# Kernel tuning notes

Measured on AMD Instinct MI355X. Metric: run time of the kernel, lower is better.

The kernel has to match this reference:

```python
import jax, jax.numpy as jnp
import numpy as np

D, H, O, E, TOPK = 1024, 4096, 1024, 8, 2
B, L = 2, 2048
ROUTE_SCALE = 1.0


def setup_inputs() -> dict:
    key = jax.random.key(0)
    ks = jax.random.split(key, 7)
    # xavier-uniform bound for gate weight (E, D)
    gb = float(np.sqrt(6.0 / (E + D)))
    return {
        "x": jax.random.normal(ks[0], (B, L, D), dtype=jnp.float32),
        "gate_w": jax.random.uniform(ks[1], (E, D), jnp.float32, -gb, gb),
        "gate_b": jnp.zeros((E,), jnp.float32),
        "w1": jax.random.normal(ks[2], (E, D, H), jnp.float32) * 0.02,
        "b1": jnp.zeros((E, H), jnp.float32),
        "w2": jax.random.normal(ks[3], (E, H, O), jnp.float32) * 0.02,
        "b2": jnp.zeros((E, O), jnp.float32),
    }


def reference(x, gate_w, gate_b, w1, b1, w2, b2):
    Bb, Ll, Dd = x.shape
    N = Bb * Ll
    x_flat = x.reshape(N, Dd)  # (N, D)

    # ---- Gate: softmax router + top-k ----
    logits = x_flat @ gate_w.T + gate_b              # (N, E)
    probs = jax.nn.softmax(logits * ROUTE_SCALE, axis=-1)
    topk_vals, topk_idx = jax.lax.top_k(probs, TOPK)  # (N, K)

    # dense gate: zeros except selected experts keep their prob
    dense_gate = jnp.zeros((N, E), probs.dtype).at[
        jnp.arange(N)[:, None], topk_idx
    ].set(topk_vals)                                  # (N, E)

    # ---- Experts (vectorized over E; gate weights are exactly zero for
    #      non-selected experts, so the combine reproduces the sparse
    #      gather-MLP-scatter math of the original loop) ----
    h = jax.nn.relu(jnp.einsum("nd,edh->neh", x_flat, w1) + b1)  # (N, E, H)
    y = jnp.einsum("neh,eho->neo", h, w2) + b2                   # (N, E, O)
    out_flat = jnp.einsum("ne,neo->no", dense_gate, y)           # (N, O)

    return out_flat.reshape(Bb, Ll, O)
```

## Files before the change

### kernel.cpp

```cpp
#include <hip/hip_runtime.h>
#include <hip/hip_bf16.h>
#include <stdint.h>

#define NTOK 4096
#define DDIM 1024
#define HDIM 4096
#define ODIM 1024
#define NEXP 8
#define BM 256
#define BN 256
#define BK 64
#define CAPROWS (NTOK * 2 + NEXP * BM)
#define MAXTILES (CAPROWS / BM)

typedef float f32x4_t __attribute__((ext_vector_type(4)));
typedef short bf16x8_t __attribute__((ext_vector_type(8)));
using bf16_t = __hip_bfloat16;

#define S_BARRIER()                         \
  do {                                      \
    __builtin_amdgcn_sched_barrier(0);      \
    __builtin_amdgcn_s_barrier();           \
    __builtin_amdgcn_sched_barrier(0);      \
  } while (0)
#define WAIT_LGKM0()                                  \
  do {                                                \
    asm volatile("s_waitcnt lgkmcnt(0)" ::: "memory");\
    __builtin_amdgcn_sched_barrier(0);                \
  } while (0)
#define WAIT_VMCNT(n)                                       \
  do {                                                      \
    asm volatile("s_waitcnt vmcnt(" #n ")" ::: "memory");   \
    __builtin_amdgcn_sched_barrier(0);                      \
  } while (0)

__device__ __forceinline__ void gll16(const void* g, void* l) {
  __builtin_amdgcn_global_load_lds(
      (__attribute__((address_space(1))) void*)(void*)g,
      (__attribute__((address_space(3))) void*)l, 16, 0, 0);
}

__global__ __launch_bounds__(256) void gate_kernel(
    const float* __restrict__ x, const float* __restrict__ gw,
    const float* __restrict__ gb, int* __restrict__ top_idx,
    float* __restrict__ top_val, int* __restrict__ counts) {
  int n = blockIdx.x * 4 + (threadIdx.x >> 6);
  int l = threadIdx.x & 63;
  const float4* xv = (const float4*)(x + (size_t)n * DDIM);
  float4 xs[4];
#pragma unroll
  for (int j = 0; j < 4; ++j) xs[j] = xv[l + 64 * j];
  float part[NEXP];
#pragma unroll
  for (int e = 0; e < NEXP; ++e) {
    const float4* wv = (const float4*)(gw + (size_t)e * DDIM);
    float s = 0.f;
#pragma unroll
    for (int j = 0; j < 4; ++j) {
      float4 w4 = wv[l + 64 * j];
      s += xs[j].x * w4.x + xs[j].y * w4.y + xs[j].z * w4.z + xs[j].w * w4.w;
    }
    part[e] = s;
  }
#pragma unroll
  for (int off = 32; off > 0; off >>= 1)
#pragma unroll
    for (int e = 0; e < NEXP; ++e) part[e] += __shfl_xor(part[e], off, 64);

  float m = -1e30f;
#pragma unroll
  for (int e = 0; e < NEXP; ++e) { part[e] += gb[e]; m = fmaxf(m, part[e]); }
  float ssum = 0.f;
#pragma unroll
  for (int e = 0; e < NEXP; ++e) { part[e] = expf(part[e] - m); ssum += part[e]; }
  int i0 = 0; float v0 = part[0];
#pragma unroll
  for (int e = 1; e < NEXP; ++e) if (part[e] > v0) { v0 = part[e]; i0 = e; }
  int i1 = -1; float v1 = -1e30f;
#pragma unroll
  for (int e = 0; e < NEXP; ++e) if (e != i0 && part[e] > v1) { v1 = part[e]; i1 = e; }
  if (l == 0) {
    float inv = 1.f / ssum;
    top_idx[n * 2] = i0; top_idx[n * 2 + 1] = i1;
    top_val[n * 2] = v0 * inv; top_val[n * 2 + 1] = v1 * inv;
    atomicAdd(&counts[i0], 1); atomicAdd(&counts[i1], 1);
  }
}

__global__ void plan_kernel(const int* __restrict__ counts, int* __restrict__ offs,
                            int* __restrict__ tile_e, int* __restrict__ tile_r) {
  if (threadIdx.x != 0 || blockIdx.x != 0) return;
  int off = 0, t = 0;
  for (int e = 0; e < NEXP; ++e) {
    offs[e] = off;
    int padded = ((counts[e] + BM - 1) / BM) * BM;
    for (int r = 0; r < padded; r += BM) { tile_e[t] = e; tile_r[t] = off + r; ++t; }
    off += padded;
  }
  offs[NEXP] = off;
  for (; t < MAXTILES; ++t) { tile_e[t] = -1; tile_r[t] = 0; }
}

__global__ __launch_bounds__(128) void gather_kernel(
    const float* __restrict__ x, const int* __restrict__ top_idx,
    const int* __restrict__ offs, int* __restrict__ cursors,
    int* __restrict__ slot_for, bf16_t* __restrict__ Xg) {
  int a = blockIdx.x;
  __shared__ int s_slot;
  if (threadIdx.x == 0) {
    int e = top_idx[a];
    int pos = atomicAdd(&cursors[e], 1);
    int slot = offs[e] + pos;
    slot_for[a] = slot;
    s_slot = slot;
  }
  __syncthreads();
  int slot = s_slot;
  int n = a >> 1;
  const float4* xv = (const float4*)(x + (size_t)n * DDIM);
  float4 a0 = xv[threadIdx.x * 2], a1 = xv[threadIdx.x * 2 + 1];
  __align__(16) bf16_t tmp[8] = {
      __float2bfloat16(a0.x), __float2bfloat16(a0.y),
      __float2bfloat16(a0.z), __float2bfloat16(a0.w),
      __float2bfloat16(a1.x), __float2bfloat16(a1.y),
      __float2bfloat16(a1.z), __float2bfloat16(a1.w)};
  *(uint4*)(Xg + (size_t)slot * DDIM + threadIdx.x * 8) = *(const uint4*)tmp;
}

__global__ __launch_bounds__(256) void convT_kernel(
    const float* __restrict__ src, bf16_t* __restrict__ dst, int R, int C) {
  __shared__ float tile[64][65];
  int e = blockIdx.z;
  int c0 = blockIdx.x * 64, r0 = blockIdx.y * 64;
  const float* s = src + ((size_t)e * R + r0) * C + c0;
  int tc = threadIdx.x & 63, tr = threadIdx.x >> 6;
#pragma unroll
  for (int p = 0; p < 16; ++p) {
    int r = tr + p * 4;
    tile[r][tc] = s[(size_t)r * C + tc];
  }
  __syncthreads();
  bf16_t* dcol = dst + ((size_t)e * C + c0) * R + r0;
  int t = threadIdx.x;
#pragma unroll
  for (int it = 0; it < 2; ++it) {
    int c = (t >> 3) + it * 32;
    int r8 = (t & 7) * 8;
    __align__(16) bf16_t v[8];
#pragma unroll
    for (int j = 0; j < 8; ++j) v[j] = __float2bfloat16(tile[r8 + j][c]);
    *(uint4*)(dcol + (size_t)c * R + r8) = *(const uint4*)v;
  }
}

template <int KTOT, int NTOT, int WHICH>
__global__ __launch_bounds__(512, 2) void gemm8_kernel(
    const bf16_t* __restrict__ A, const bf16_t* __restrict__ Bt,
    const float* __restrict__ bias, void* __restrict__ Cout,
    const int* __restrict__ tile_e, const int* __restrict__ tile_r) {
  constexpr int NCOL = NTOT / BN;
  int nwg = gridDim.x;
  int bid = blockIdx.x;
  int q = nwg >> 3, rr = nwg & 7;
  int xcd = bid & 7, pos = bid >> 3;
  int swz = (xcd < rr ? xcd * (q + 1) : rr * (q + 1) + (xcd - rr) * q) + pos;
  int ty = swz / NCOL, tx = swz % NCOL;

  int e = tile_e[ty];
  if (e < 0) return;
  int row0 = tile_r[ty];
  int n0 = tx * BN;

  __shared__ char smem[131072];
  int tid = threadIdx.x;
  int w = tid >> 6, l = tid & 63;
  int wm = w >> 2, wn = w & 3;
  int lrow = l & 15, lk = l >> 4;

  const bf16_t* Ab = A + (size_t)row0 * KTOT;
  const bf16_t* Bb = Bt + ((size_t)e * NTOT + n0) * KTOT;

  int sidx0 = tid, sidx1 = 512 + tid;
  int sr0 = sidx0 >> 3, sc0 = (sidx0 & 7) ^ (sr0 & 7);
  int sr1 = sidx1 >> 3, sc1 = (sidx1 & 7) ^ (sr1 & 7);

  auto stageA = [&](int kt, int h, int d) {
    char* lb = smem + d * 32768 + h * 16384;
    const bf16_t* g = Ab + (size_t)(h * 128) * KTOT + kt * BK;
    gll16(g + (size_t)sr0 * KTOT + sc0 * 8, lb + sidx0 * 16);
    gll16(g + (size_t)sr1 * KTOT + sc1 * 8, lb + sidx1 * 16);
  };
  auto stageB = [&](int kt, int h, int d) {
    char* lb = smem + 65536 + d * 32768 + h * 16384;
    const bf16_t* g = Bb + (size_t)(h * 128) * KTOT + kt * BK;
    gll16(g + (size_t)sr0 * KTOT + sc0 * 8, lb + sidx0 * 16);
    gll16(g + (size_t)sr1 * KTOT + sc1 * 8, lb + sidx1 * 16);
  };

  int abase = (wm * 128 + lrow) * 128;
  int bbase = (wn * 64 + lrow) * 128;
  int p0 = ((lk) ^ (lrow & 7)) * 16;
  int p1 = ((4 + lk) ^ (lrow & 7)) * 16;

  f32x4_t acc[8][4];
#pragma unroll
  for (int m = 0; m < 8; ++m)
#pragma unroll
    for (int n = 0; n < 4; ++n) acc[m][n] = (f32x4_t){0.f, 0.f, 0.f, 0.f};

  const int NKT = KTOT / BK;

  stageA(0, 0, 0); stageA(0, 1, 0);
  stageB(0, 0, 0); stageB(0, 1, 0);
  stageA(1, 0, 1); stageA(1, 1, 1);
  WAIT_VMCNT(4);
  S_BARRIER();

  for (int t = 0; t < NKT; ++t) {
    int d = t & 1;
    const char* Ad = smem + d * 32768;
    const char* Bd = smem + 65536 + d * 32768;
    bf16x8_t ak0[8], ak1[8], bv[4];
#pragma unroll
    for (int m = 0; m < 8; ++m)
      ak0[m] = *(const bf16x8_t*)(Ad + abase + m * 2048 + p0);
#pragma unroll
    for (int n = 0; n < 4; ++n)
      bv[n] = *(const bf16x8_t*)(Bd + bbase + n * 2048 + p0);
    if (t + 1 < NKT) stageB(t + 1, 0, d ^ 1);
    S_BARRIER();
    WAIT_LGKM0();
    __builtin_amdgcn_s_setprio(1);
#pragma unroll
    for (int m = 0; m < 4; ++m)
#pragma unroll
      for (int n = 0; n < 4; ++n)
        acc[m][n] = __builtin_amdgcn_mfma_f32_16x16x32_bf16(ak0[m], bv[n], acc[m][n], 0, 0, 0);
    __builtin_amdgcn_s_setprio(0);
    S_BARRIER();
#pragma unroll
    for (int m = 0; m < 8; ++m)
      ak1[m] = *(const bf16x8_t*)(Ad + abase + m * 2048 + p1);
    if (t + 1 < NKT) stageB(t + 1, 1, d ^ 1);
    S_BARRIER();
    WAIT_LGKM0();
    __builtin_amdgcn_s_setprio(1);
#pragma unroll
    for (int m = 4; m < 8; ++m)
#pragma unroll
      for (int n = 0; n < 4; ++n)
        acc[m][n] = __builtin_amdgcn_mfma_f32_16x16x32_bf16(ak0[m], bv[n], acc[m][n], 0, 0, 0);
    __builtin_amdgcn_s_setprio(0);
    S_BARRIER();
#pragma unroll
    for (int n = 0; n < 4; ++n)
      bv[n] = *(const bf16x8_t*)(Bd + bbase + n * 2048 + p1);
    if (t + 2 < NKT) stageA(t + 2, 0, d);
    S_BARRIER();
    WAIT_LGKM0();
    __builtin_amdgcn_s_setprio(1);
#pragma unroll
    for (int m = 0; m < 4; ++m)
#pragma unroll
      for (int n = 0; n < 4; ++n)
        acc[m][n] = __builtin_amdgcn_mfma_f32_16x16x32_bf16(ak1[m], bv[n], acc[m][n], 0, 0, 0);
    __builtin_amdgcn_s_setprio(0);
    S_BARRIER();
    if (t + 2 < NKT) {
      stageA(t + 2, 1, d);
      WAIT_VMCNT(4);
    } else {
      WAIT_VMCNT(0);
    }
    S_BARRIER();
    __builtin_amdgcn_s_setprio(1);
#pragma unroll
    for (int m = 4; m < 8; ++m)
#pragma unroll
      for (int n = 0; n < 4; ++n)
        acc[m][n] = __builtin_amdgcn_mfma_f32_16x16x32_bf16(ak1[m], bv[n], acc[m][n], 0, 0, 0);
    __builtin_amdgcn_s_setprio(0);
    S_BARRIER();
  }

#pragma unroll
  for (int n = 0; n < 4; ++n) {
    int col = n0 + wn * 64 + n * 16 + lrow;
    float bb = bias[e * NTOT + col];
#pragma unroll
    for (int m = 0; m < 8; ++m) {
      size_t rb = (size_t)row0 + wm * 128 + m * 16 + lk * 4;
#pragma unroll
      for (int i = 0; i < 4; ++i) {
        float v = acc[m][n][i] + bb;
        if (WHICH == 1) {
          v = v > 0.f ? v : 0.f;
          ((bf16_t*)Cout)[(rb + i) * NTOT + col] = __float2bfloat16(v);
        } else {
          ((float*)Cout)[(rb + i) * NTOT + col] = v;
        }
      }
    }
  }
}

__global__ __launch_bounds__(256) void combine_kernel(
    const float* __restrict__ Y, const int* __restrict__ slot_for,
    const float* __restrict__ top_val, float* __restrict__ out) {
  int n = blockIdx.x;
  int s0 = slot_for[n * 2], s1 = slot_for[n * 2 + 1];
  float v0 = top_val[n * 2], v1 = top_val[n * 2 + 1];
  int t = threadIdx.x;
  float4 a = ((const float4*)(Y + (size_t)s0 * ODIM))[t];
  float4 b = ((const float4*)(Y + (size_t)s1 * ODIM))[t];
  float4 r;
  r.x = v0 * a.x + v1 * b.x;
  r.y = v0 * a.y + v1 * b.y;
  r.z = v0 * a.z + v1 * b.z;
  r.w = v0 * a.w + v1 * b.w;
  ((float4*)(out + (size_t)n * ODIM))[t] = r;
}

__global__ void zero_meta_kernel(int* p) {
  if (threadIdx.x < 16) p[threadIdx.x] = 0;
}

extern "C" void kernel_launch(void* const* d_in, const int* in_sizes, int n_in,
                              void* d_out, int out_size, void* d_ws, size_t ws_size,
                              hipStream_t stream) {
  const float* x  = (const float*)d_in[0];
  const float* gw = (const float*)d_in[1];
  const float* gb = (const float*)d_in[2];
  const float* w1 = (const float*)d_in[3];
  const float* b1 = (const float*)d_in[4];
  const float* w2 = (const float*)d_in[5];
  const float* b2 = (const float*)d_in[6];
  float* out = (float*)d_out;

  char* ws = (char*)d_ws;
  size_t off = 0;
  auto alloc = [&](size_t bytes) {
    void* p = ws + off;
    off = (off + bytes + 255) & ~(size_t)255;
    return p;
  };
  bf16_t* w1T = (bf16_t*)alloc((size_t)NEXP * HDIM * DDIM * 2);
  bf16_t* w2T = (bf16_t*)alloc((size_t)NEXP * ODIM * HDIM * 2);
  bf16_t* Xg  = (bf16_t*)alloc((size_t)CAPROWS * DDIM * 2);
  bf16_t* Hb  = (bf16_t*)alloc((size_t)CAPROWS * HDIM * 2);
  int* counts  = (int*)alloc(64);
  int* cursors = counts + 8;
  int* offs    = (int*)alloc(64);
  int* tile_e  = (int*)alloc(MAXTILES * 4);
  int* tile_r  = (int*)alloc(MAXTILES * 4);
  int* top_idx = (int*)alloc((size_t)NTOK * 2 * 4);
  float* top_val = (float*)alloc((size_t)NTOK * 2 * 4);
  int* slot_for = (int*)alloc((size_t)NTOK * 2 * 4);
  float* Yb = (float*)w1T;

  hipLaunchKernelGGL(zero_meta_kernel, dim3(1), dim3(64), 0, stream, counts);
  hipMemsetAsync(Xg, 0, (size_t)CAPROWS * DDIM * 2, stream);
  hipLaunchKernelGGL(convT_kernel, dim3(HDIM / 64, DDIM / 64, NEXP), dim3(256), 0,
                     stream, w1, w1T, DDIM, HDIM);
  hipLaunchKernelGGL(convT_kernel, dim3(ODIM / 64, HDIM / 64, NEXP), dim3(256), 0,
                     stream, w2, w2T, HDIM, ODIM);
  hipLaunchKernelGGL(gate_kernel, dim3(NTOK / 4), dim3(256), 0, stream,
                     x, gw, gb, top_idx, top_val, counts);
  hipLaunchKernelGGL(plan_kernel, dim3(1), dim3(1), 0, stream,
                     counts, offs, tile_e, tile_r);
  hipLaunchKernelGGL(gather_kernel, dim3(NTOK * 2), dim3(128), 0, stream,
                     x, top_idx, offs, cursors, slot_for, Xg);
  hipLaunchKernelGGL((gemm8_kernel<DDIM, HDIM, 1>),
                     dim3((HDIM / BN) * MAXTILES), dim3(512), 0, stream,
                     Xg, w1T, b1, Hb, tile_e, tile_r);
  hipLaunchKernelGGL((gemm8_kernel<HDIM, ODIM, 2>),
                     dim3((ODIM / BN) * MAXTILES), dim3(512), 0, stream,
                     Hb, w2T, b2, Yb, tile_e, tile_r);
  hipLaunchKernelGGL(combine_kernel, dim3(NTOK), dim3(256), 0, stream,
                     Yb, slot_for, top_val, out);
}
```

Baseline: 736.2 us.

## Restructure GEMM pipeline prefetch, stage epilogue through LDS, drop Xg memset

The GEMM main loop now prefetches both A and B two K-steps ahead and loads all fragments for a step up front, instead of interleaving B staging for the next step with compute. This removes the explicit LDS waits and reduces stalls between MFMA phases. The epilogue now writes results into shared memory and then issues coalesced 16-byte global stores, replacing scattered per-element stores. The memset of the gathered-input buffer is dropped, so padding rows hold stale data. Those rows only produce outputs that are never read, but the change relies on that.

```diff
diff --git a/kernel.cpp b/kernel.cpp
--- a/kernel.cpp
+++ b/kernel.cpp
@@ -22,11 +22,6 @@
     __builtin_amdgcn_sched_barrier(0);      \
     __builtin_amdgcn_s_barrier();           \
     __builtin_amdgcn_sched_barrier(0);      \
-  } while (0)
-#define WAIT_LGKM0()                                  \
-  do {                                                \
-    asm volatile("s_waitcnt lgkmcnt(0)" ::: "memory");\
-    __builtin_amdgcn_sched_barrier(0);                \
   } while (0)
 #define WAIT_VMCNT(n)                                       \
   do {                                                      \
@@ -213,62 +208,61 @@
   stageA(0, 0, 0); stageA(0, 1, 0);
   stageB(0, 0, 0); stageB(0, 1, 0);
   stageA(1, 0, 1); stageA(1, 1, 1);
-  WAIT_VMCNT(4);
+  stageB(1, 0, 1); stageB(1, 1, 1);
+  WAIT_VMCNT(8);
   S_BARRIER();
 
   for (int t = 0; t < NKT; ++t) {
     int d = t & 1;
     const char* Ad = smem + d * 32768;
     const char* Bd = smem + 65536 + d * 32768;
-    bf16x8_t ak0[8], ak1[8], bv[4];
+    bf16x8_t ak0[8], ak1[8], bv0[4], bv1[4];
+    bool pre = (t + 2 < NKT);
 #pragma unroll
     for (int m = 0; m < 8; ++m)
       ak0[m] = *(const bf16x8_t*)(Ad + abase + m * 2048 + p0);
 #pragma unroll
     for (int n = 0; n < 4; ++n)
-      bv[n] = *(const bf16x8_t*)(Bd + bbase + n * 2048 + p0);
-    if (t + 1 < NKT) stageB(t + 1, 0, d ^ 1);
-    S_BARRIER();
-    WAIT_LGKM0();
-    __builtin_amdgcn_s_setprio(1);
-#pragma unroll
-    for (int m = 0; m < 4; ++m)
-#pragma unroll
-      for (int n = 0; n < 4; ++n)
-        acc[m][n] = __builtin_amdgcn_mfma_f32_16x16x32_bf16(ak0[m], bv[n], acc[m][n], 0, 0, 0);
-    __builtin_amdgcn_s_setprio(0);
-    S_BARRIER();
+      bv0[n] = *(const bf16x8_t*)(Bd + bbase + n * 2048 + p0);
 #pragma unroll
     for (int m = 0; m < 8; ++m)
       ak1[m] = *(const bf16x8_t*)(Ad + abase + m * 2048 + p1);
-    if (t + 1 < NKT) stageB(t + 1, 1, d ^ 1);
-    S_BARRIER();
-    WAIT_LGKM0();
+    S_BARRIER();
     __builtin_amdgcn_s_setprio(1);
 #pragma unroll
+    for (int m = 0; m < 4; ++m)
+#pragma unroll
+      for (int n = 0; n < 4; ++n)
+        acc[m][n] = __builtin_amdgcn_mfma_f32_16x16x32_bf16(ak0[m], bv0[n], acc[m][n], 0, 0, 0);
+    __builtin_amdgcn_s_setprio(0);
+    S_BARRIER();
+    if (pre) stageA(t + 2, 0, d);
+    S_BARRIER();
+    __builtin_amdgcn_s_setprio(1);
+#pragma unroll
     for (int m = 4; m < 8; ++m)
 #pragma unroll
       for (int n = 0; n < 4; ++n)
-        acc[m][n] = __builtin_amdgcn_mfma_f32_16x16x32_bf16(ak0[m], bv[n], acc[m][n], 0, 0, 0);
+        acc[m][n] = __builtin_amdgcn_mfma_f32_16x16x32_bf16(ak0[m], bv0[n], acc[m][n], 0, 0, 0);
     __builtin_amdgcn_s_setprio(0);
     S_BARRIER();
 #pragma unroll
     for (int n = 0; n < 4; ++n)
-      bv[n] = *(const bf16x8_t*)(Bd + bbase + n * 2048 + p1);
-    if (t + 2 < NKT) stageA(t + 2, 0, d);
-    S_BARRIER();
-    WAIT_LGKM0();
+      bv1[n] = *(const bf16x8_t*)(Bd + bbase + n * 2048 + p1);
+    if (pre) stageA(t + 2, 1, d);
+    S_BARRIER();
     __builtin_amdgcn_s_setprio(1);
 #pragma unroll
     for (int m = 0; m < 4; ++m)
 #pragma unroll
       for (int n = 0; n < 4; ++n)
-        acc[m][n] = __builtin_amdgcn_mfma_f32_16x16x32_bf16(ak1[m], bv[n], acc[m][n], 0, 0, 0);
+        acc[m][n] = __builtin_amdgcn_mfma_f32_16x16x32_bf16(ak1[m], bv1[n], acc[m][n], 0, 0, 0);
     __builtin_amdgcn_s_setprio(0);
     S_BARRIER();
-    if (t + 2 < NKT) {
-      stageA(t + 2, 1, d);
-      WAIT_VMCNT(4);
+    if (pre) {
+      stageB(t + 2, 0, d);
+      stageB(t + 2, 1, d);
+      WAIT_VMCNT(8);
     } else {
       WAIT_VMCNT(0);
     }
@@ -278,27 +272,60 @@
     for (int m = 4; m < 8; ++m)
 #pragma unroll
       for (int n = 0; n < 4; ++n)
-        acc[m][n] = __builtin_amdgcn_mfma_f32_16x16x32_bf16(ak1[m], bv[n], acc[m][n], 0, 0, 0);
+        acc[m][n] = __builtin_amdgcn_mfma_f32_16x16x32_bf16(ak1[m], bv1[n], acc[m][n], 0, 0, 0);
     __builtin_amdgcn_s_setprio(0);
     S_BARRIER();
   }
 
-#pragma unroll
-  for (int n = 0; n < 4; ++n) {
-    int col = n0 + wn * 64 + n * 16 + lrow;
-    float bb = bias[e * NTOT + col];
-#pragma unroll
-    for (int m = 0; m < 8; ++m) {
-      size_t rb = (size_t)row0 + wm * 128 + m * 16 + lk * 4;
-#pragma unroll
-      for (int i = 0; i < 4; ++i) {
-        float v = acc[m][n][i] + bb;
-        if (WHICH == 1) {
+  if (WHICH == 1) {
+#pragma unroll
+    for (int n = 0; n < 4; ++n) {
+      int col = wn * 64 + n * 16 + lrow;
+      float bb = bias[e * NTOT + n0 + col];
+#pragma unroll
+      for (int m = 0; m < 8; ++m) {
+        int rb = wm * 128 + m * 16 + lk * 4;
+#pragma unroll
+        for (int i = 0; i < 4; ++i) {
+          float v = acc[m][n][i] + bb;
           v = v > 0.f ? v : 0.f;
-          ((bf16_t*)Cout)[(rb + i) * NTOT + col] = __float2bfloat16(v);
-        } else {
-          ((float*)Cout)[(rb + i) * NTOT + col] = v;
+          *(bf16_t*)(smem + (size_t)(rb + i) * 512 + col * 2) = __float2bfloat16(v);
         }
+      }
+    }
+    S_BARRIER();
+#pragma unroll
+    for (int p = 0; p < 16; ++p) {
+      int idx = p * 512 + tid;
+      int row = idx >> 5, ch = idx & 31;
+      uint4 v = *(const uint4*)(smem + (size_t)row * 512 + ch * 16);
+      *(uint4*)((char*)Cout + ((size_t)(row0 + row) * NTOT + n0) * 2 + ch * 16) = v;
+    }
+  } else {
+#pragma unroll
+    for (int h = 0; h < 2; ++h) {
+      if (h) S_BARRIER();
+      if (wm == h) {
+#pragma unroll
+        for (int n = 0; n < 4; ++n) {
+          int col = wn * 64 + n * 16 + lrow;
+          float bb = bias[e * NTOT + n0 + col];
+#pragma unroll
+          for (int m = 0; m < 8; ++m) {
+            int rb = m * 16 + lk * 4;
+#pragma unroll
+            for (int i = 0; i < 4; ++i)
+              *(float*)(smem + (size_t)(rb + i) * 1024 + col * 4) = acc[m][n][i] + bb;
+          }
+        }
+      }
+      S_BARRIER();
+#pragma unroll
+      for (int p = 0; p < 16; ++p) {
+        int idx = p * 512 + tid;
+        int row = idx >> 6, ch = idx & 63;
+        uint4 v = *(const uint4*)(smem + (size_t)row * 1024 + ch * 16);
+        *(uint4*)((char*)Cout + ((size_t)(row0 + h * 128 + row) * NTOT + n0) * 4 + ch * 16) = v;
       }
     }
   }
@@ -359,7 +386,6 @@
   float* Yb = (float*)w1T;
 
   hipLaunchKernelGGL(zero_meta_kernel, dim3(1), dim3(64), 0, stream, counts);
-  hipMemsetAsync(Xg, 0, (size_t)CAPROWS * DDIM * 2, stream);
   hipLaunchKernelGGL(convT_kernel, dim3(HDIM / 64, DDIM / 64, NEXP), dim3(256), 0,
                      stream, w1, w1T, DDIM, HDIM);
   hipLaunchKernelGGL(convT_kernel, dim3(ODIM / 64, HDIM / 64, NEXP), dim3(256), 0,
```

Result: no change. 736.0 us (-0.0%).
